# Kernel tuning notes

Measured on AMD Instinct MI355X. Metric: run time of the kernel, lower is better.

## Reference

```python
import jax, jax.numpy as jnp
import numpy as np


def setup_inputs() -> dict:
    key = jax.random.key(0)
    ks = jax.random.split(key, 13)
    B, T, D = 512, 256, 64
    H, G = 256, 192          # encoder hidden, lifted dim
    L = D + G                # ldim = 256
    s = lambda n: 1.0 / np.sqrt(n)
    return {
        "x": jax.random.normal(ks[0], (B, T, D), jnp.float32),
        "u": jax.random.normal(ks[1], (B, T, D), jnp.float32),
        "Wx1": jax.random.normal(ks[2], (D, H), jnp.float32) * s(D),
        "bx1": jax.random.normal(ks[3], (H,), jnp.float32) * 0.01,
        "Wx2": jax.random.normal(ks[4], (H, H), jnp.float32) * s(H),
        "bx2": jax.random.normal(ks[5], (H,), jnp.float32) * 0.01,
        "Wx3": jax.random.normal(ks[6], (H, G), jnp.float32) * s(H),
        "Wu1": jax.random.normal(ks[7], (D, H), jnp.float32) * s(D),
        "bu1": jax.random.normal(ks[8], (H,), jnp.float32) * 0.01,
        "Wu2": jax.random.normal(ks[9], (H, G), jnp.float32) * s(H),
        "WB": jax.random.normal(ks[10], (D + G, L), jnp.float32) * s(D + G),
        "WK": jax.random.normal(ks[11], (L, L), jnp.float32) * s(L),
        "bK": jax.random.normal(ks[12], (L,), jnp.float32) * 0.01,
        "n_shifts": 256,
    }


def reference(x, u, Wx1, bx1, Wx2, bx2, Wx3, Wu1, bu1, Wu2, WB, WK, bK, n_shifts):
    x = x[:, :n_shifts, :]
    u = u[:, :n_shifts, :]
    # encoder_x: relu(Linear) -> relu(Linear) -> Linear(no bias), dropout p=0 is identity
    g = jnp.maximum(x @ Wx1 + bx1, 0.0)
    g = jnp.maximum(g @ Wx2 + bx2, 0.0)
    g = g @ Wx3
    y = jnp.concatenate([x, g], axis=-1)          # [B, T, ldim]
    # encoder_u: relu(Linear) -> Linear(no bias)
    v = jnp.maximum(u @ Wu1 + bu1, 0.0) @ Wu2
    uu = jnp.concatenate([u, v], axis=-1)         # [B, T, D+G]
    Bu = uu @ WB                                  # [B, T, ldim]
    # Koopman linear recurrence: y_{t+1} = K y_t + bK + Bu_t
    y0 = y[:, 0, :]                               # [B, ldim]

    def step(carry, bu_t):
        y_next = carry @ WK + bK + bu_t
        return y_next, y_next

    _, ys = jax.lax.scan(step, y0, jnp.swapaxes(Bu[:, :-1, :], 0, 1))  # [T-1, B, ldim]
    y_pred = jnp.concatenate([y0[:, None, :], jnp.swapaxes(ys, 0, 1)], axis=1)
    return (y, y_pred)
```

## Files before the change

### kernel.cpp

```cpp
#include <hip/hip_runtime.h>
#include <hip/hip_bf16.h>

#define MM 131072

typedef __attribute__((ext_vector_type(8))) short short8;
typedef __attribute__((ext_vector_type(4))) float f32x4;

#define GLP(p) (const __attribute__((address_space(1))) void*)(p)
#define LDSP(p) (__attribute__((address_space(3))) void*)(p)

static __device__ __forceinline__ unsigned short f2bf(float f) {
    union { float f; unsigned int u; } v; v.f = f;
    unsigned int r = v.u + 0x7FFF + ((v.u >> 16) & 1);
    return (unsigned short)(r >> 16);
}
static __device__ __forceinline__ float bf2f(unsigned short h) {
    union { float f; unsigned int u; } v; v.u = ((unsigned int)h) << 16;
    return v.f;
}

__global__ __launch_bounds__(256) void prepA(
    const float* __restrict__ x, const float* __restrict__ u,
    __hip_bfloat16* __restrict__ xb, __hip_bfloat16* __restrict__ ub,
    float* __restrict__ y,
// ... 69 lines not shown
            __syncthreads();
            #pragma unroll
            for (int kk = 0; kk < 16; ++kk) {
                const float4 a4 = *(const float4*)&As[kk][ty * 4];
                const float4 w4 = *(const float4*)&Ws[kk][tx * 4];
                const float av[4] = {a4.x, a4.y, a4.z, a4.w};
                const float wv[4] = {w4.x, w4.y, w4.z, w4.w};
                #pragma unroll
                for (int i = 0; i < 4; ++i)
                    #pragma unroll
                    for (int j = 0; j < 4; ++j)
                        acc[i][j] += av[i] * wv[j];
            }
            __syncthreads();
        }
        #pragma unroll
        for (int i = 0; i < 4; ++i)
            #pragma unroll
            for (int j = 0; j < 4; ++j)
                C[(size_t)(row0 + ty * 4 + i) * 256 + col0 + tx * 4 + j] = acc[i][j];
    }
}

struct G5 { const float* a[5]; const float* b[5]; float* c[5]; };

__global__ __launch_bounds__(256) void wgemm(G5 P)
{
    __shared__ __align__(16) float As[16][68];
    __shared__ __align__(16) float Ws[16][64];

    const int e  = blockIdx.x >> 4;
    const int tl = blockIdx.x & 15;
    const float* A = P.a[e];
    const float* W = P.b[e];
    float*       C = P.c[e];
    const int row0 = (tl >> 2) * 64;
    const int col0 = (tl & 3) * 64;

    const int tx = threadIdx.x & 15;
    const int ty = threadIdx.x >> 4;

    float acc[4][4] = {};

    for (int k0 = 0; k0 < 256; k0 += 16) {
        {
            const int kk = threadIdx.x & 15;
            const int r  = threadIdx.x >> 4;
            #pragma unroll
            for (int rr = 0; rr < 4; ++rr)
                As[kk][r + rr * 16] = A[(size_t)(row0 + r + rr * 16) * 256 + k0 + kk];
        }
        {
            const int n  = threadIdx.x & 63;
            const int kz = threadIdx.x >> 6;
            #pragma unroll
            for (int kq = 0; kq < 4; ++kq) {
                const int kk = kz + kq * 4;
                Ws[kk][n] = W[(size_t)(k0 + kk) * 256 + col0 + n];
            }
        }
        __syncthreads();
        #pragma unroll
        for (int kk = 0; kk < 16; ++kk) {
            const float4 a4 = *(const float4*)&As[kk][ty * 4];
            const float4 w4 = *(const float4*)&Ws[kk][tx * 4];
            const float av[4] = {a4.x, a4.y, a4.z, a4.w};
            const float wv[4] = {w4.x, w4.y, w4.z, w4.w};
            #pragma unroll
            for (int i = 0; i < 4; ++i)
                #pragma unroll
                for (int j = 0; j < 4; ++j)
                    acc[i][j] += av[i] * wv[j];
        }
        __syncthreads();
    }

    #pragma unroll
    for (int i = 0; i < 4; ++i)
        #pragma unroll
        for (int j = 0; j < 4; ++j)
            C[(size_t)(row0 + ty * 4 + i) * 256 + col0 + tx * 4 + j] = acc[i][j];
}

__global__ __launch_bounds__(512) void ffC(
    const __hip_bfloat16* __restrict__ x_bf,
    const __hip_bfloat16* __restrict__ u_bf,
    const __hip_bfloat16* __restrict__ Wx1T, const float* __restrict__ bx1,
    const __hip_bfloat16* __restrict__ Wx2T, const float* __restrict__ bx2,
    const __hip_bfloat16* __restrict__ Wx3T,
    const __hip_bfloat16* __restrict__ Wu1T, const float* __restrict__ bu1,
    const __hip_bfloat16* __restrict__ Wu2T,
    float* __restrict__ y, __hip_bfloat16* __restrict__ vout,
    const float* __restrict__ WB, const float* __restrict__ WBW,
    const float* __restrict__ WBW2, const float* __restrict__ WBW3,
    __hip_bfloat16* __restrict__ T4,
    const float* __restrict__ bK, const float* __restrict__ WK,
    const float* __restrict__ W2f, const float* __restrict__ W3f,
    float* __restrict__ cK4)
{
    __shared__ __align__(16) __hip_bfloat16 I[128 * 256];
    __shared__ __align__(16) __hip_bfloat16 Bs[256 * 128];
    __shared__ __align__(16) __hip_bfloat16 As[128 * 64];

    const int tid  = threadIdx.x;

    if (blockIdx.x >= 2048) {
        if (blockIdx.x < 2560) {
            const int o = (blockIdx.x - 2048) * 512 + tid;
            const int n = o >> 10;
            const int rem = o & 1023;
            const int j = rem >> 8, k = rem & 255;
            const float* src = (j == 0) ? WB : (j == 1) ? WBW : (j == 2) ? WBW2 : WBW3;
            ((unsigned short*)T4)[o] = f2bf(src[(size_t)k * 256 + n]);
        } else {
            if (tid < 256) {
                const int col = tid;
                float s = bK[col];
                for (int k = 0; k < 256; ++k)
                    s += bK[k] * (WK[(size_t)k * 256 + col] + W2f[(size_t)k * 256 + col]
                                  + W3f[(size_t)k * 256 + col]);
                cK4[col] = s;
            }
        }
        return;
    }

    const bool isx = blockIdx.x < 1024;
    const __hip_bfloat16* in  = isx ? x_bf : u_bf;
    const __hip_bfloat16* W1T = isx ? Wx1T : Wu1T;
    const float*          b1  = isx ? bx1  : bu1;
    const int lane = tid & 63;
    const int wid  = tid >> 6;
    const int wm   = wid & 1;
    const int wn   = wid >> 1;
    const int row0 = (blockIdx.x & 1023) * 128;
    const int rlow = lane & 15;
    const int c    = lane >> 4;

    f32x4 acc[4][4];
    #pragma unroll
    for (int mi = 0; mi < 4; ++mi)
        #pragma unroll
        for (int ni = 0; ni < 4; ++ni)
            acc[mi][ni] = {0.f, 0.f, 0.f, 0.f};

    {
        #pragma unroll
        for (int r = 0; r < 2; ++r) {
            const int i = r * 512 + tid;
            const int row = i >> 3;
            const int cl  = (i & 7) ^ (row & 7);
            __builtin_amdgcn_global_load_lds(
                GLP(in + (size_t)(row0 + row) * 64 + cl * 8),
                LDSP(As + i * 8), 16, 0, 0);
        }
        #pragma unroll
        for (int r = 0; r < 4; ++r) {
            const int i = r * 512 + tid;
            const int row = i >> 3;
            const int cl  = (i & 7) ^ (row & 7);
            __builtin_amdgcn_global_load_lds(
                GLP(W1T + (size_t)row * 64 + cl * 8),
                LDSP(Bs + i * 8), 16, 0, 0);
        }
        __syncthreads();
        #pragma unroll
        for (int k0 = 0; k0 < 64; k0 += 32) {
            short8 af[4], bfr[4];
            #pragma unroll
            for (int mi = 0; mi < 4; ++mi) {
                const int row  = wm * 64 + mi * 16 + rlow;
                const int phys = ((k0 >> 3) + c) ^ (row & 7);
                af[mi] = *(const short8*)((const char*)As + row * 128 + phys * 16);
            }
            #pragma unroll
            for (int ni = 0; ni < 4; ++ni) {
                const int row  = wn * 64 + ni * 16 + rlow;
                const int phys = ((k0 >> 3) + c) ^ (row & 7);
                bfr[ni] = *(const short8*)((const char*)Bs + row * 128 + phys * 16);
            }
            #pragma unroll
            for (int mi = 0; mi < 4; ++mi)
                #pragma unroll
                for (int ni = 0; ni < 4; ++ni)
                    acc[mi][ni] = __builtin_amdgcn_mfma_f32_16x16x32_bf16(
                        af[mi], bfr[ni], acc[mi][ni], 0, 0, 0);
        }
        __syncthreads();
        #pragma unroll
        for (int ni = 0; ni < 4; ++ni) {
            const int col = wn * 64 + ni * 16 + rlow;
            const float bv = b1[col];
            #pragma unroll
            for (int q = 0; q < 4; ++q)
                #pragma unroll
                for (int mi = 0; mi < 4; ++mi) {
                    const int row = wm * 64 + mi * 16 + c * 4 + q;
                    const int byte = (row * 512 + col * 2) ^ ((row & 7) << 4);
                    *(unsigned short*)((char*)I + byte) = f2bf(fmaxf(acc[mi][ni][q] + bv, 0.f));
                }
        }
        __syncthreads();
    }

    if (isx) {
        #pragma unroll
        for (int mi = 0; mi < 4; ++mi)
            #pragma unroll
            for (int ni = 0; ni < 4; ++ni)
                acc[mi][ni] = {0.f, 0.f, 0.f, 0.f};

        for (int half = 0; half < 2; ++half) {
            const int k0b = half * 128;
            #pragma unroll
            for (int r = 0; r < 8; ++r) {
                const int i = r * 512 + tid;
                const int row = i >> 4;
                const int cl  = (i & 15) ^ (row & 7);
                __builtin_amdgcn_global_load_lds(
                    GLP(Wx2T + (size_t)row * 256 + k0b + cl * 8),
                    LDSP(Bs + i * 8), 16, 0, 0);
            }
            __syncthreads();
            #pragma unroll
            for (int k0l = 0; k0l < 128; k0l += 32) {
                short8 af[4], bfr[4];
                #pragma unroll
                for (int mi = 0; mi < 4; ++mi) {
                    const int row = wm * 64 + mi * 16 + rlow;
                    const int off = (row * 512 + (k0b + k0l) * 2 + c * 16) ^ ((row & 7) << 4);
                    af[mi] = *(const short8*)((const char*)I + off);
                }
                #pragma unroll
                for (int ni = 0; ni < 4; ++ni) {
                    const int row  = wn * 64 + ni * 16 + rlow;
                    const int phys = ((k0l >> 3) + c) ^ (row & 7);
                    bfr[ni] = *(const short8*)((const char*)Bs + row * 256 + phys * 16);
                }
                #pragma unroll
                for (int mi = 0; mi < 4; ++mi)
                    #pragma unroll
                    for (int ni = 0; ni < 4; ++ni)
                        acc[mi][ni] = __builtin_amdgcn_mfma_f32_16x16x32_bf16(
                            af[mi], bfr[ni], acc[mi][ni], 0, 0, 0);
            }
            __syncthreads();
        }
        #pragma unroll
        for (int ni = 0; ni < 4; ++ni) {
            const int col = wn * 64 + ni * 16 + rlow;
            const float bv = bx2[col];
            #pragma unroll
            for (int q = 0; q < 4; ++q)
                #pragma unroll
                for (int mi = 0; mi < 4; ++mi) {
                    const int row = wm * 64 + mi * 16 + c * 4 + q;
                    const int byte = (row * 512 + col * 2) ^ ((row & 7) << 4);
                    *(unsigned short*)((char*)I + byte) = f2bf(fmaxf(acc[mi][ni][q] + bv, 0.f));
                }
        }
        __syncthreads();
    }

    const __hip_bfloat16* WfT = isx ? Wx3T : Wu2T;
    f32x4 a3[4][3];
    #pragma unroll
    for (int mi = 0; mi < 4; ++mi)
        #pragma unroll
        for (int ni = 0; ni < 3; ++ni)
            a3[mi][ni] = {0.f, 0.f, 0.f, 0.f};

    for (int half = 0; half < 2; ++half) {
        const int k0b = half * 128;
        #pragma unroll
        for (int r = 0; r < 6; ++r) {
            const int i = r * 512 + tid;
            const int row = i >> 4;
            const int cl  = (i & 15) ^ (row & 7);
            __builtin_amdgcn_global_load_lds(
                GLP(WfT + (size_t)row * 256 + k0b + cl * 8),
                LDSP(Bs + i * 8), 16, 0, 0);
        }
        __syncthreads();
        #pragma unroll
        for (int k0l = 0; k0l < 128; k0l += 32) {
            short8 af[4], bfr[3];
            #pragma unroll
            for (int mi = 0; mi < 4; ++mi) {
                const int row = wm * 64 + mi * 16 + rlow;
                const int off = (row * 512 + (k0b + k0l) * 2 + c * 16) ^ ((row & 7) << 4);
                af[mi] = *(const short8*)((const char*)I + off);
            }
            #pragma unroll
            for (int ni = 0; ni < 3; ++ni) {
                const int row  = wn * 48 + ni * 16 + rlow;
                const int phys = ((k0l >> 3) + c) ^ (row & 7);
                bfr[ni] = *(const short8*)((const char*)Bs + row * 256 + phys * 16);
            }
            #pragma unroll
            for (int mi = 0; mi < 4; ++mi)
                #pragma unroll
                for (int ni = 0; ni < 3; ++ni)
                    a3[mi][ni] = __builtin_amdgcn_mfma_f32_16x16x32_bf16(
                        af[mi], bfr[ni], a3[mi][ni], 0, 0, 0);
        }
        __syncthreads();
    }
    #pragma unroll
    for (int ni = 0; ni < 3; ++ni) {
        const int col = wn * 48 + ni * 16 + rlow;
        #pragma unroll
        for (int mi = 0; mi < 4; ++mi)
            #pragma unroll
            for (int q = 0; q < 4; ++q) {
                const int row = row0 + wm * 64 + mi * 16 + c * 4 + q;
                if (isx) y[(size_t)row * 256 + 64 + col] = a3[mi][ni][q];
                else     ((unsigned short*)vout)[(size_t)row * 192 + col] = f2bf(a3[mi][ni][q]);
            }
    }
}

__global__ __launch_bounds__(256) void d4gS(
    const __hip_bfloat16* __restrict__ u_bf, const __hip_bfloat16* __restrict__ v,
    const __hip_bfloat16* __restrict__ WBT4, const float* __restrict__ cK4,
    float* __restrict__ yp,
    const __hip_bfloat16* __restrict__ WBT, const float* __restrict__ bK,
    float* __restrict__ stash)
{
    __shared__ __align__(16) __hip_bfloat16 As[132 * 32];
    __shared__ __align__(16) __hip_bfloat16 Bs[4][128 * 32];

    const int tid  = threadIdx.x;

    if (blockIdx.x >= 2048) {
        float* uuL = (float*)As;
        const int b = blockIdx.x - 2048;
        #pragma unroll
        for (int p = 0; p < 3; ++p) {
            float val;
            if (tid < 64) val = bf2f(((const unsigned short*)u_bf)[((size_t)b * 256 + p) * 64 + tid]);
            else          val = bf2f(((const unsigned short*)v)[((size_t)b * 256 + p) * 192 + tid - 64]);
            uuL[p * 256 + tid] = val;
        }
        __syncthreads();
        const int col = tid;
        float a0 = bK[col], a1 = a0, a2 = a0;
        for (int k = 0; k < 256; ++k) {
            const float w = bf2f(((const unsigned short*)WBT)[(size_t)col * 256 + k]);
            a0 += uuL[0 * 256 + k] * w;
            a1 += uuL[1 * 256 + k] * w;
            a2 += uuL[2 * 256 + k] * w;
        }
        stash[((size_t)b * 3 + 0) * 256 + col] = a0;
        stash[((size_t)b * 3 + 1) * 256 + col] = a1;
        stash[((size_t)b * 3 + 2) * 256 + col] = a2;
        return;
    }

    const int lane = tid & 63;
    const int wid  = tid >> 6;
    const int wm   = wid & 1;
    const int wn   = wid >> 1;
    const int row0 = (blockIdx.x >> 1) * 128;
    const int col0 = (blockIdx.x & 1) * 128;
    const int rlow = lane & 15;
    const int c    = lane >> 4;

    f32x4 acc[4][4];
    #pragma unroll
    for (int mi = 0; mi < 4; ++mi)
        #pragma unroll
        for (int ni = 0; ni < 4; ++ni)
            acc[mi][ni] = {0.f, 0.f, 0.f, 0.f};

    for (int kl = 0; kl < 256; kl += 32) {
        const __hip_bfloat16* Ab; int Al, kk;
        if (kl < 64) { Ab = u_bf; Al = 64;  kk = kl; }
        else         { Ab = v;    Al = 192; kk = kl - 64; }

        #pragma unroll
        for (int r = 0; r < 3; ++r) {
            const int i = r * 256 + tid;
            if (i < 528) {
                const int row = i >> 2;
                const int cl  = (i & 3) ^ ((row >> 1) & 3);
                int srow = row0 - 4 + row;
                if (srow < 0) srow = 0;
                __builtin_amdgcn_global_load_lds(
                    GLP(Ab + (size_t)srow * Al + kk + cl * 8),
                    LDSP(As + i * 8), 16, 0, 0);
            }
        }
        #pragma unroll
        for (int r = 0; r < 8; ++r) {
            const int i = r * 256 + tid;
            const int j = i >> 9;
            const int s = i & 511;
            const int row = s >> 2;
            const int cl  = (s & 3) ^ ((row >> 1) & 3);
            __builtin_amdgcn_global_load_lds(
                GLP(WBT4 + (size_t)(col0 + row) * 1024 + j * 256 + kl + cl * 8),
                LDSP(&Bs[0][0] + i * 8), 16, 0, 0);
        }
        __syncthreads();

        #pragma unroll
        for (int j = 0; j < 4; ++j) {
            short8 bfr[4];
            #pragma unroll
            for (int ni = 0; ni < 4; ++ni) {
                const int row  = wn * 64 + ni * 16 + rlow;
                const int phys = c ^ ((row >> 1) & 3);
                bfr[ni] = *(const short8*)((const char*)Bs[j] + row * 64 + phys * 16);
            }
            #pragma unroll
            for (int mi = 0; mi < 4; ++mi) {
                const int prow = wm * 64 + mi * 16 + rlow + 3 - j;
                const int phys = c ^ ((prow >> 1) & 3);
                const short8 af = *(const short8*)((const char*)As + prow * 64 + phys * 16);
                #pragma unroll
                for (int ni = 0; ni < 4; ++ni)
                    acc[mi][ni] = __builtin_amdgcn_mfma_f32_16x16x32_bf16(
                        af, bfr[ni], acc[mi][ni], 0, 0, 0);
            }
        }
        __syncthreads();
    }

    const int q4 = lane >> 4;
    #pragma unroll
    for (int ni = 0; ni < 4; ++ni) {
        const int col = col0 + wn * 64 + ni * 16 + rlow;
        const float bv = cK4[col];
        #pragma unroll
        for (int mi = 0; mi < 4; ++mi) {
            #pragma unroll
            for (int q = 0; q < 4; ++q) {
                const int row = row0 + wm * 64 + mi * 16 + q4 * 4 + q;
                if ((row & 255) >= 4)
                    yp[(size_t)row * 256 + col] = acc[mi][ni][q] + bv;
            }
        }
    }
}

static __device__ __forceinline__ void gather_frags(
    const float* __restrict__ M, int col0, int rlow, int kg,
    short8 (&wh)[2][8], short8 (&wl)[2][8])
{
    #pragma unroll
    for (int tile = 0; tile < 2; ++tile) {
        const int col = col0 + tile * 16 + rlow;
        for (int kc = 0; kc < 8; ++kc) {
            const int k0 = kc * 32 + kg * 8;
            short8 h, l;
            for (int i = 0; i < 8; ++i) {
                const float w = M[(size_t)(k0 + i) * 256 + col];
                const unsigned short hb = f2bf(w);
                h[i] = (short)hb;
                l[i] = (short)f2bf(w - bf2f(hb));
            }
            wh[tile][kc] = h;
            wl[tile][kc] = l;
        }
    }
}

__global__ __launch_bounds__(512, 1) void scan4(
    const float* __restrict__ WK, const float* __restrict__ W4,
    const float* __restrict__ stash,
    const float* __restrict__ y, float* __restrict__ yp)
{
    __shared__ __align__(16) __hip_bfloat16 cbuf[2][2][16 * 256];

    const int tid  = threadIdx.x;
    const int lane = tid & 63;
    const int wid  = tid >> 6;
    const int b0   = blockIdx.x * 4;
    const int col0 = wid * 32;
    const int rlow = lane & 15;
    const int kg   = lane >> 4;
    const int rswz = (rlow & 7) << 4;

    #pragma unroll
    for (int e = 0; e < 2; ++e) {
        const int idx = tid * 2 + e;
        const int br  = idx >> 8;
        const int cc  = idx & 255;
        const float v = y[(size_t)(b0 + br) * 65536 + cc];
        yp[(size_t)(b0 + br) * 65536 + cc] = v;
        const unsigned short hb = f2bf(v);
        const unsigned short lb = f2bf(v - bf2f(hb));
        const int byte = (br * 512 + cc * 2) ^ ((br & 7) << 4);
        *(unsigned short*)((char*)&cbuf[0][0][0] + byte) = hb;
        *(unsigned short*)((char*)&cbuf[0][1][0] + byte) = lb;
    }
    __syncthreads();

    short8 wh[2][8], wl[2][8];
    gather_frags(WK, col0, rlow, kg, wh, wl);

    for (int p = 1; p < 4; ++p) {
        f32x4 aHH[2], aHL[2], aLH[2], bHH[2], bHL[2], bLH[2];
        #pragma unroll
        for (int tile = 0; tile < 2; ++tile) {
            aHH[tile] = {0.f,0.f,0.f,0.f}; aHL[tile] = {0.f,0.f,0.f,0.f}; aLH[tile] = {0.f,0.f,0.f,0.f};
            bHH[tile] = {0.f,0.f,0.f,0.f}; bHL[tile] = {0.f,0.f,0.f,0.f}; bLH[tile] = {0.f,0.f,0.f,0.f};
        }
        const char* hbase = (const char*)&cbuf[0][0][0];
        const char* lbase = (const char*)&cbuf[0][1][0];
        #pragma unroll
        for (int kc = 0; kc < 4; ++kc) {
            const int off = (rlow * 512 + kg * 16 + kc * 64) ^ rswz;
            const short8 ah = *(const short8*)(hbase + off);
            const short8 al = *(const short8*)(lbase + off);
            aHH[0] = __builtin_amdgcn_mfma_f32_16x16x32_bf16(ah, wh[0][kc], aHH[0], 0, 0, 0);
            aHH[1] = __builtin_amdgcn_mfma_f32_16x16x32_bf16(ah, wh[1][kc], aHH[1], 0, 0, 0);
            aHL[0] = __builtin_amdgcn_mfma_f32_16x16x32_bf16(ah, wl[0][kc], aHL[0], 0, 0, 0);
            aHL[1] = __builtin_amdgcn_mfma_f32_16x16x32_bf16(ah, wl[1][kc], aHL[1], 0, 0, 0);
            aLH[0] = __builtin_amdgcn_mfma_f32_16x16x32_bf16(al, wh[0][kc], aLH[0], 0, 0, 0);
            aLH[1] = __builtin_amdgcn_mfma_f32_16x16x32_bf16(al, wh[1][kc], aLH[1], 0, 0, 0);
        }
        #pragma unroll
        for (int kc = 4; kc < 8; ++kc) {
            const int off = (rlow * 512 + kg * 16 + kc * 64) ^ rswz;
            const short8 ah = *(const short8*)(hbase + off);
            const short8 al = *(const short8*)(lbase + off);
            bHH[0] = __builtin_amdgcn_mfma_f32_16x16x32_bf16(ah, wh[0][kc], bHH[0], 0, 0, 0);
            bHH[1] = __builtin_amdgcn_mfma_f32_16x16x32_bf16(ah, wh[1][kc], bHH[1], 0, 0, 0);
            bHL[0] = __builtin_amdgcn_mfma_f32_16x16x32_bf16(ah, wl[0][kc], bHL[0], 0, 0, 0);
            bHL[1] = __builtin_amdgcn_mfma_f32_16x16x32_bf16(ah, wl[1][kc], bHL[1], 0, 0, 0);
            bLH[0] = __builtin_amdgcn_mfma_f32_16x16x32_bf16(al, wh[0][kc], bLH[0], 0, 0, 0);
            bLH[1] = __builtin_amdgcn_mfma_f32_16x16x32_bf16(al, wh[1][kc], bLH[1], 0, 0, 0);
        }
        __builtin_amdgcn_sched_barrier(0);
        asm volatile("s_waitcnt lgkmcnt(0)" ::: "memory");
        __builtin_amdgcn_s_barrier();
        __builtin_amdgcn_sched_barrier(0);

        if (kg == p - 1) {
            #pragma unroll
            for (int tile = 0; tile < 2; ++tile) {
                const int col = col0 + tile * 16 + rlow;
                #pragma unroll
                for (int q = 0; q < 4; ++q) {
                    const float cv = stash[((size_t)(b0 + q) * 3 + (p - 1)) * 256 + col];
                    const float yv = (aHH[tile][q] + bHH[tile][q]) + (aHL[tile][q] + bHL[tile][q])
                                   + (aLH[tile][q] + bLH[tile][q]) + cv;
                    const int wr = p * 4 + q;
                    const unsigned short hb = f2bf(yv);
                    const unsigned short lb = f2bf(yv - bf2f(hb));
                    const int byte = (wr * 512 + col * 2) ^ ((wr & 7) << 4);
                    *(unsigned short*)((char*)&cbuf[0][0][0] + byte) = hb;
                    *(unsigned short*)((char*)&cbuf[0][1][0] + byte) = lb;
                    yp[(size_t)(b0 + q) * 65536 + (size_t)p * 256 + col] = yv;
                }
            }
        }
        __builtin_amdgcn_sched_barrier(0);
        asm volatile("s_waitcnt lgkmcnt(0)" ::: "memory");
        __builtin_amdgcn_s_barrier();
        __builtin_amdgcn_sched_barrier(0);
    }

    gather_frags(W4, col0, rlow, kg, wh, wl);

    float dv[2][4];
    #pragma unroll
    for (int tile = 0; tile < 2; ++tile) {
        const int col = col0 + tile * 16 + rlow;
        #pragma unroll
        for (int q = 0; q < 4; ++q)
            dv[tile][q] = yp[(size_t)(b0 + q) * 65536 + (size_t)(4 + kg) * 256 + col];
    }

    int cur = 0;
    for (int s = 0; s < 63; ++s) {
        const int tb = 4 + s * 4;

        float dn[2][4];
        if (s < 62) {
            #pragma unroll
            for (int tile = 0; tile < 2; ++tile) {
                const int col = col0 + tile * 16 + rlow;
                #pragma unroll
                for (int q = 0; q < 4; ++q)
                    dn[tile][q] = yp[(size_t)(b0 + q) * 65536
                                     + (size_t)(tb + 4 + kg) * 256 + col];
            }
        }

        f32x4 aHH[2], aHL[2], aLH[2], bHH[2], bHL[2], bLH[2];
        #pragma unroll
        for (int tile = 0; tile < 2; ++tile) {
            aHH[tile] = {0.f,0.f,0.f,0.f}; aHL[tile] = {0.f,0.f,0.f,0.f}; aLH[tile] = {0.f,0.f,0.f,0.f};
            bHH[tile] = {0.f,0.f,0.f,0.f}; bHL[tile] = {0.f,0.f,0.f,0.f}; bLH[tile] = {0.f,0.f,0.f,0.f};
        }
        const char* hbase = (const char*)&cbuf[cur][0][0];
        const char* lbase = (const char*)&cbuf[cur][1][0];
        #pragma unroll
        for (int kc = 0; kc < 4; ++kc) {
            const int off = (rlow * 512 + kg * 16 + kc * 64) ^ rswz;
            const short8 ah = *(const short8*)(hbase + off);
            const short8 al = *(const short8*)(lbase + off);
            aHH[0] = __builtin_amdgcn_mfma_f32_16x16x32_bf16(ah, wh[0][kc], aHH[0], 0, 0, 0);
            aHH[1] = __builtin_amdgcn_mfma_f32_16x16x32_bf16(ah, wh[1][kc], aHH[1], 0, 0, 0);
            aHL[0] = __builtin_amdgcn_mfma_f32_16x16x32_bf16(ah, wl[0][kc], aHL[0], 0, 0, 0);
            aHL[1] = __builtin_amdgcn_mfma_f32_16x16x32_bf16(ah, wl[1][kc], aHL[1], 0, 0, 0);
            aLH[0] = __builtin_amdgcn_mfma_f32_16x16x32_bf16(al, wh[0][kc], aLH[0], 0, 0, 0);
            aLH[1] = __builtin_amdgcn_mfma_f32_16x16x32_bf16(al, wh[1][kc], aLH[1], 0, 0, 0);
        }
        #pragma unroll
        for (int kc = 4; kc < 8; ++kc) {
            const int off = (rlow * 512 + kg * 16 + kc * 64) ^ rswz;
            const short8 ah = *(const short8*)(hbase + off);
            const short8 al = *(const short8*)(lbase + off);
            bHH[0] = __builtin_amdgcn_mfma_f32_16x16x32_bf16(ah, wh[0][kc], bHH[0], 0, 0, 0);
            bHH[1] = __builtin_amdgcn_mfma_f32_16x16x32_bf16(ah, wh[1][kc], bHH[1], 0, 0, 0);
            bHL[0] = __builtin_amdgcn_mfma_f32_16x16x32_bf16(ah, wl[0][kc], bHL[0], 0, 0, 0);
            bHL[1] = __builtin_amdgcn_mfma_f32_16x16x32_bf16(ah, wl[1][kc], bHL[1], 0, 0, 0);
            bLH[0] = __builtin_amdgcn_mfma_f32_16x16x32_bf16(al, wh[0][kc], bLH[0], 0, 0, 0);
            bLH[1] = __builtin_amdgcn_mfma_f32_16x16x32_bf16(al, wh[1][kc], bLH[1], 0, 0, 0);
        }

        char* whb = (char*)&cbuf[cur ^ 1][0][0];
        char* wlb = (char*)&cbuf[cur ^ 1][1][0];
        #pragma unroll
        for (int tile = 0; tile < 2; ++tile) {
            const int col = col0 + tile * 16 + rlow;
            #pragma unroll
            for (int q = 0; q < 4; ++q) {
                const int row = kg * 4 + q;
                const float yv = (aHH[tile][q] + bHH[tile][q]) + (aHL[tile][q] + bHL[tile][q])
                               + (aLH[tile][q] + bLH[tile][q]) + dv[tile][q];
                const unsigned short hb = f2bf(yv);
                const unsigned short lb = f2bf(yv - bf2f(hb));
                const int byte = (row * 512 + col * 2) ^ ((row & 7) << 4);
                *(unsigned short*)(whb + byte) = hb;
                *(unsigned short*)(wlb + byte) = lb;
                yp[(size_t)(b0 + q) * 65536 + (size_t)(tb + kg) * 256 + col] = yv;
            }
        }
        if (s < 62) {
            #pragma unroll
            for (int tile = 0; tile < 2; ++tile)
                #pragma unroll
                for (int q = 0; q < 4; ++q)
                    dv[tile][q] = dn[tile][q];
        }

        __builtin_amdgcn_sched_barrier(0);
        asm volatile("s_waitcnt lgkmcnt(0)" ::: "memory");
        __builtin_amdgcn_s_barrier();
        __builtin_amdgcn_sched_barrier(0);
        cur ^= 1;
    }
}

extern "C" void kernel_launch(void* const* d_in, const int* in_sizes, int n_in,
                              void* d_out, int out_size, void* d_ws, size_t ws_size,
                              hipStream_t stream)
{
    const float* x   = (const float*)d_in[0];
    const float* u   = (const float*)d_in[1];
    const float* Wx1 = (const float*)d_in[2];
    const float* bx1 = (const float*)d_in[3];
    const float* Wx2 = (const float*)d_in[4];
    const float* bx2 = (const float*)d_in[5];
    const float* Wx3 = (const float*)d_in[6];
    const float* Wu1 = (const float*)d_in[7];
    const float* bu1 = (const float*)d_in[8];
    const float* Wu2 = (const float*)d_in[9];
    const float* WB  = (const float*)d_in[10];
    const float* WK  = (const float*)d_in[11];
    const float* bK  = (const float*)d_in[12];

    float* y  = (float*)d_out;
    float* yp = y + (size_t)MM * 256;

    char* ws = (char*)d_ws;
    __hip_bfloat16* x_bf = (__hip_bfloat16*)(ws);
    __hip_bfloat16* u_bf = (__hip_bfloat16*)(ws + 16777216);
    __hip_bfloat16* wTb  = (__hip_bfloat16*)(ws + 33554432);
    __hip_bfloat16* Wx1T = wTb;
    __hip_bfloat16* Wx2T = wTb + 16384;
    __hip_bfloat16* Wx3T = wTb + 81920;
    __hip_bfloat16* Wu1T = wTb + 131072;
    __hip_bfloat16* Wu2T = wTb + 147456;
    __hip_bfloat16* WBT  = wTb + 196608;
    __hip_bfloat16* t2   = (__hip_bfloat16*)(ws + 34078720);
    float* W2f   = (float*)(ws + 101187584);
    float* W3f   = (float*)(ws + 101449728);
    float* W4f   = (float*)(ws + 101711872);
    float* WBWf  = (float*)(ws + 101974016);
    float* WBW2f = (float*)(ws + 102236160);
    float* WBW3f = (float*)(ws + 102498304);
    __hip_bfloat16* WBT4 = (__hip_bfloat16*)(ws + 102760448);
    float* cK4   = (float*)(ws + 103284736);
    float* stash = (float*)(ws + 103285760);

    prepA<<<17440, dim3(256), 0, stream>>>(x, u, x_bf, u_bf, y,
        Wx1, Wx2, Wx3, Wu1, Wu2, WB,
        Wx1T, Wx2T, Wx3T, Wu1T, Wu2T, WBT,
        WK, WB, W2f, WBWf);

    {
        G5 L2 = {{W2f, W2f, WBWf, WBWf, nullptr},
                 {WK, W2f, WK, W2f, nullptr},
                 {W3f, W4f, WBW2f, WBW3f, nullptr}};
        wgemm<<<64, dim3(256), 0, stream>>>(L2);
    }

    ffC<<<2561, dim3(512), 0, stream>>>(x_bf, u_bf,
        Wx1T, bx1, Wx2T, bx2, Wx3T, Wu1T, bu1, Wu2T,
        y, t2,
        WB, WBWf, WBW2f, WBW3f, WBT4,
        bK, WK, W2f, W3f, cK4);

    d4gS<<<2560, dim3(256), 0, stream>>>(u_bf, t2, WBT4, cK4, yp, WBT, bK, stash);

    scan4<<<128, dim3(512), 0, stream>>>(WK, W4f, stash, y, yp);
}
```

Baseline: 392.7 us.

## Overlap x-encoder MLP with Koopman scan by moving it into scan kernel

```diff
diff --git a/kernel.cpp b/kernel.cpp
--- a/kernel.cpp
+++ b/kernel.cpp
@@ -175,7 +175,204 @@
             C[(size_t)(row0 + ty * 4 + i) * 256 + col0 + tx * 4 + j] = acc[i][j];
 }
 
-__global__ __launch_bounds__(512) void ffC(
+static __device__ void ffx_impl(
+    const __hip_bfloat16* __restrict__ x_bf,
+    const __hip_bfloat16* __restrict__ W1T, const float* __restrict__ b1,
+    const __hip_bfloat16* __restrict__ W2T, const float* __restrict__ b2,
+    const __hip_bfloat16* __restrict__ W3T,
+    float* __restrict__ y, int row0, int rs, char* smem, int tid)
+{
+    __hip_bfloat16* I  = (__hip_bfloat16*)smem;
+    __hip_bfloat16* Bs = (__hip_bfloat16*)(smem + 65536);
+    __hip_bfloat16* As = (__hip_bfloat16*)(smem + 131072);
+
+    const int lane = tid & 63;
+    const int wid  = tid >> 6;
+    const int wm   = wid & 1;
+    const int wn   = wid >> 1;
+    const int rlow = lane & 15;
+    const int c    = lane >> 4;
+
+    f32x4 acc[4][4];
+    #pragma unroll
+    for (int mi = 0; mi < 4; ++mi)
+        #pragma unroll
+        for (int ni = 0; ni < 4; ++ni)
+            acc[mi][ni] = {0.f, 0.f, 0.f, 0.f};
+
+    {
+        #pragma unroll
+        for (int r = 0; r < 2; ++r) {
+            const int i = r * 512 + tid;
+            const int row = i >> 3;
+            const int cl  = (i & 7) ^ (row & 7);
+            __builtin_amdgcn_global_load_lds(
+                GLP(x_bf + (size_t)(row0 + row * rs) * 64 + cl * 8),
+                LDSP(As + i * 8), 16, 0, 0);
+        }
+        #pragma unroll
+        for (int r = 0; r < 4; ++r) {
+            const int i = r * 512 + tid;
+            const int row = i >> 3;
+            const int cl  = (i & 7) ^ (row & 7);
+            __builtin_amdgcn_global_load_lds(
+                GLP(W1T + (size_t)row * 64 + cl * 8),
+                LDSP(Bs + i * 8), 16, 0, 0);
+        }
+        __syncthreads();
+        #pragma unroll
+        for (int k0 = 0; k0 < 64; k0 += 32) {
+            short8 af[4], bfr[4];
+            #pragma unroll
+            for (int mi = 0; mi < 4; ++mi) {
+                const int row  = wm * 64 + mi * 16 + rlow;
+                const int phys = ((k0 >> 3) + c) ^ (row & 7);
+                af[mi] = *(const short8*)((const char*)As + row * 128 + phys * 16);
+            }
+            #pragma unroll
+            for (int ni = 0; ni < 4; ++ni) {
+                const int row  = wn * 64 + ni * 16 + rlow;
+                const int phys = ((k0 >> 3) + c) ^ (row & 7);
+                bfr[ni] = *(const short8*)((const char*)Bs + row * 128 + phys * 16);
+            }
+            #pragma unroll
+            for (int mi = 0; mi < 4; ++mi)
+                #pragma unroll
+                for (int ni = 0; ni < 4; ++ni)
+                    acc[mi][ni] = __builtin_amdgcn_mfma_f32_16x16x32_bf16(
+                        af[mi], bfr[ni], acc[mi][ni], 0, 0, 0);
+        }
+        __syncthreads();
+        #pragma unroll
+        for (int ni = 0; ni < 4; ++ni) {
+            const int col = wn * 64 + ni * 16 + rlow;
+            const float bv = b1[col];
+            #pragma unroll
+            for (int q = 0; q < 4; ++q)
+                #pragma unroll
+                for (int mi = 0; mi < 4; ++mi) {
+                    const int row = wm * 64 + mi * 16 + c * 4 + q;
+                    const int byte = (row * 512 + col * 2) ^ ((row & 7) << 4);
+                    *(unsigned short*)((char*)I + byte) = f2bf(fmaxf(acc[mi][ni][q] + bv, 0.f));
+                }
+        }
+        __syncthreads();
+    }
+
+    #pragma unroll
+    for (int mi = 0; mi < 4; ++mi)
+        #pragma unroll
+        for (int ni = 0; ni < 4; ++ni)
+            acc[mi][ni] = {0.f, 0.f, 0.f, 0.f};
+
+    for (int half = 0; half < 2; ++half) {
+        const int k0b = half * 128;
+        #pragma unroll
+        for (int r = 0; r < 8; ++r) {
+            const int i = r * 512 + tid;
+            const int row = i >> 4;
+            const int cl  = (i & 15) ^ (row & 7);
+            __builtin_amdgcn_global_load_lds(
+                GLP(W2T + (size_t)row * 256 + k0b + cl * 8),
+                LDSP(Bs + i * 8), 16, 0, 0);
+        }
+        __syncthreads();
+        #pragma unroll
+        for (int k0l = 0; k0l < 128; k0l += 32) {
+            short8 af[4], bfr[4];
+            #pragma unroll
+            for (int mi = 0; mi < 4; ++mi) {
+                const int row = wm * 64 + mi * 16 + rlow;
+                const int off = (row * 512 + (k0b + k0l) * 2 + c * 16) ^ ((row & 7) << 4);
+                af[mi] = *(const short8*)((const char*)I + off);
+            }
+            #pragma unroll
+            for (int ni = 0; ni < 4; ++ni) {
+                const int row  = wn * 64 + ni * 16 + rlow;
+                const int phys = ((k0l >> 3) + c) ^ (row & 7);
+                bfr[ni] = *(const short8*)((const char*)Bs + row * 256 + phys * 16);
+            }
+            #pragma unroll
+            for (int mi = 0; mi < 4; ++mi)
+                #pragma unroll
+                for (int ni = 0; ni < 4; ++ni)
+                    acc[mi][ni] = __builtin_amdgcn_mfma_f32_16x16x32_bf16(
+                        af[mi], bfr[ni], acc[mi][ni], 0, 0, 0);
+        }
+        __syncthreads();
+    }
+    #pragma unroll
+    for (int ni = 0; ni < 4; ++ni) {
+        const int col = wn * 64 + ni * 16 + rlow;
+        const float bv = b2[col];
+        #pragma unroll
+        for (int q = 0; q < 4; ++q)
+            #pragma unroll
+            for (int mi = 0; mi < 4; ++mi) {
+                const int row = wm * 64 + mi * 16 + c * 4 + q;
+                const int byte = (row * 512 + col * 2) ^ ((row & 7) << 4);
+                *(unsigned short*)((char*)I + byte) = f2bf(fmaxf(acc[mi][ni][q] + bv, 0.f));
+            }
+    }
+    __syncthreads();
+
+    f32x4 a3[4][3];
+    #pragma unroll
+    for (int mi = 0; mi < 4; ++mi)
+        #pragma unroll
+        for (int ni = 0; ni < 3; ++ni)
+            a3[mi][ni] = {0.f, 0.f, 0.f, 0.f};
+
+    for (int half = 0; half < 2; ++half) {
+        const int k0b = half * 128;
+        #pragma unroll
+        for (int r = 0; r < 6; ++r) {
+            const int i = r * 512 + tid;
+            const int row = i >> 4;
+            const int cl  = (i & 15) ^ (row & 7);
+            __builtin_amdgcn_global_load_lds(
+                GLP(W3T + (size_t)row * 256 + k0b + cl * 8),
+                LDSP(Bs + i * 8), 16, 0, 0);
+        }
+        __syncthreads();
+        #pragma unroll
+        for (int k0l = 0; k0l < 128; k0l += 32) {
+            short8 af[4], bfr[3];
+            #pragma unroll
+            for (int mi = 0; mi < 4; ++mi) {
+                const int row = wm * 64 + mi * 16 + rlow;
+                const int off = (row * 512 + (k0b + k0l) * 2 + c * 16) ^ ((row & 7) << 4);
+                af[mi] = *(const short8*)((const char*)I + off);
+            }
+            #pragma unroll
+            for (int ni = 0; ni < 3; ++ni) {
+                const int row  = wn * 48 + ni * 16 + rlow;
+                const int phys = ((k0l >> 3) + c) ^ (row & 7);
+                bfr[ni] = *(const short8*)((const char*)Bs + row * 256 + phys * 16);
+            }
+            #pragma unroll
+            for (int mi = 0; mi < 4; ++mi)
+                #pragma unroll
+                for (int ni = 0; ni < 3; ++ni)
+                    a3[mi][ni] = __builtin_amdgcn_mfma_f32_16x16x32_bf16(
+                        af[mi], bfr[ni], a3[mi][ni], 0, 0, 0);
+        }
+        __syncthreads();
+    }
+    #pragma unroll
+    for (int ni = 0; ni < 3; ++ni) {
+        const int col = wn * 48 + ni * 16 + rlow;
+        #pragma unroll
+        for (int mi = 0; mi < 4; ++mi)
+            #pragma unroll
+            for (int q = 0; q < 4; ++q) {
+                const int row = row0 + (wm * 64 + mi * 16 + c * 4 + q) * rs;
+                y[(size_t)row * 256 + 64 + col] = a3[mi][ni][q];
+            }
+    }
+}
+
+__global__ __launch_bounds__(512) void midC(
     const __hip_bfloat16* __restrict__ x_bf,
     const __hip_bfloat16* __restrict__ u_bf,
     const __hip_bfloat16* __restrict__ Wx1T, const float* __restrict__ bx1,
@@ -191,21 +388,18 @@
     const float* __restrict__ W2f, const float* __restrict__ W3f,
     float* __restrict__ cK4)
 {
-    __shared__ __align__(16) __hip_bfloat16 I[128 * 256];
-    __shared__ __align__(16) __hip_bfloat16 Bs[256 * 128];
-    __shared__ __align__(16) __hip_bfloat16 As[128 * 64];
-
-    const int tid  = threadIdx.x;
-
-    if (blockIdx.x >= 2048) {
-        if (blockIdx.x < 2560) {
-            const int o = (blockIdx.x - 2048) * 512 + tid;
+    __shared__ __align__(16) char smem[147456];
+    const int tid = threadIdx.x;
+
+    if (blockIdx.x >= 1024) {
+        if (blockIdx.x < 1536) {
+            const int o = (blockIdx.x - 1024) * 512 + tid;
             const int n = o >> 10;
             const int rem = o & 1023;
             const int j = rem >> 8, k = rem & 255;
             const float* src = (j == 0) ? WB : (j == 1) ? WBW : (j == 2) ? WBW2 : WBW3;
             ((unsigned short*)T4)[o] = f2bf(src[(size_t)k * 256 + n]);
-        } else {
+        } else if (blockIdx.x == 1536) {
             if (tid < 256) {
                 const int col = tid;
                 float s = bK[col];
@@ -214,19 +408,23 @@
                                   + W3f[(size_t)k * 256 + col]);
                 cK4[col] = s;
             }
+        } else {
+            const int base = (blockIdx.x - 1537) * 128;
+            ffx_impl(x_bf, Wx1T, bx1, Wx2T, bx2, Wx3T, y,
+                     base * 256, 256, smem, tid);
         }
         return;
     }
 
-    const bool isx = blockIdx.x < 1024;
-    const __hip_bfloat16* in  = isx ? x_bf : u_bf;
-    const __hip_bfloat16* W1T = isx ? Wx1T : Wu1T;
-    const float*          b1  = isx ? bx1  : bu1;
+    __hip_bfloat16* I  = (__hip_bfloat16*)smem;
+    __hip_bfloat16* Bs = (__hip_bfloat16*)(smem + 65536);
+    __hip_bfloat16* As = (__hip_bfloat16*)(smem + 131072);
+
     const int lane = tid & 63;
     const int wid  = tid >> 6;
     const int wm   = wid & 1;
     const int wn   = wid >> 1;
-    const int row0 = (blockIdx.x & 1023) * 128;
+    const int row0 = blockIdx.x * 128;
     const int rlow = lane & 15;
     const int c    = lane >> 4;
 
@@ -244,7 +442,7 @@
             const int row = i >> 3;
             const int cl  = (i & 7) ^ (row & 7);
             __builtin_amdgcn_global_load_lds(
-                GLP(in + (size_t)(row0 + row) * 64 + cl * 8),
+                GLP(u_bf + (size_t)(row0 + row) * 64 + cl * 8),
                 LDSP(As + i * 8), 16, 0, 0);
         }
         #pragma unroll
@@ -253,7 +451,7 @@
             const int row = i >> 3;
             const int cl  = (i & 7) ^ (row & 7);
             __builtin_amdgcn_global_load_lds(
-                GLP(W1T + (size_t)row * 64 + cl * 8),
+                GLP(Wu1T + (size_t)row * 64 + cl * 8),
                 LDSP(Bs + i * 8), 16, 0, 0);
         }
         __syncthreads();
@@ -283,7 +481,7 @@
         #pragma unroll
         for (int ni = 0; ni < 4; ++ni) {
             const int col = wn * 64 + ni * 16 + rlow;
-            const float bv = b1[col];
+            const float bv = bu1[col];
             #pragma unroll
             for (int q = 0; q < 4; ++q)
                 #pragma unroll
@@ -296,66 +494,6 @@
         __syncthreads();
     }
 
-    if (isx) {
-        #pragma unroll
-        for (int mi = 0; mi < 4; ++mi)
-            #pragma unroll
-            for (int ni = 0; ni < 4; ++ni)
-                acc[mi][ni] = {0.f, 0.f, 0.f, 0.f};
-
-        for (int half = 0; half < 2; ++half) {
-            const int k0b = half * 128;
-            #pragma unroll
-            for (int r = 0; r < 8; ++r) {
-                const int i = r * 512 + tid;
-                const int row = i >> 4;
-                const int cl  = (i & 15) ^ (row & 7);
-                __builtin_amdgcn_global_load_lds(
-                    GLP(Wx2T + (size_t)row * 256 + k0b + cl * 8),
-                    LDSP(Bs + i * 8), 16, 0, 0);
-            }
-            __syncthreads();
-            #pragma unroll
-            for (int k0l = 0; k0l < 128; k0l += 32) {
-                short8 af[4], bfr[4];
-                #pragma unroll
-                for (int mi = 0; mi < 4; ++mi) {
-                    const int row = wm * 64 + mi * 16 + rlow;
-                    const int off = (row * 512 + (k0b + k0l) * 2 + c * 16) ^ ((row & 7) << 4);
-                    af[mi] = *(const short8*)((const char*)I + off);
-                }
-                #pragma unroll
-                for (int ni = 0; ni < 4; ++ni) {
-                    const int row  = wn * 64 + ni * 16 + rlow;
-                    const int phys = ((k0l >> 3) + c) ^ (row & 7);
-                    bfr[ni] = *(const short8*)((const char*)Bs + row * 256 + phys * 16);
-                }
-                #pragma unroll
-                for (int mi = 0; mi < 4; ++mi)
-                    #pragma unroll
-                    for (int ni = 0; ni < 4; ++ni)
-                        acc[mi][ni] = __builtin_amdgcn_mfma_f32_16x16x32_bf16(
-                            af[mi], bfr[ni], acc[mi][ni], 0, 0, 0);
-            }
-            __syncthreads();
-        }
-        #pragma unroll
-        for (int ni = 0; ni < 4; ++ni) {
-            const int col = wn * 64 + ni * 16 + rlow;
-            const float bv = bx2[col];
-            #pragma unroll
-            for (int q = 0; q < 4; ++q)
-                #pragma unroll
-                for (int mi = 0; mi < 4; ++mi) {
-                    const int row = wm * 64 + mi * 16 + c * 4 + q;
-                    const int byte = (row * 512 + col * 2) ^ ((row & 7) << 4);
-                    *(unsigned short*)((char*)I + byte) = f2bf(fmaxf(acc[mi][ni][q] + bv, 0.f));
-                }
-        }
-        __syncthreads();
-    }
-
-    const __hip_bfloat16* WfT = isx ? Wx3T : Wu2T;
     f32x4 a3[4][3];
     #pragma unroll
     for (int mi = 0; mi < 4; ++mi)
@@ -371,7 +509,7 @@
             const int row = i >> 4;
             const int cl  = (i & 15) ^ (row & 7);
             __builtin_amdgcn_global_load_lds(
-                GLP(WfT + (size_t)row * 256 + k0b + cl * 8),
+                GLP(Wu2T + (size_t)row * 256 + k0b + cl * 8),
                 LDSP(Bs + i * 8), 16, 0, 0);
         }
         __syncthreads();
@@ -407,8 +545,7 @@
             #pragma unroll
             for (int q = 0; q < 4; ++q) {
                 const int row = row0 + wm * 64 + mi * 16 + c * 4 + q;
-                if (isx) y[(size_t)row * 256 + 64 + col] = a3[mi][ni][q];
-                else     ((unsigned short*)vout)[(size_t)row * 192 + col] = f2bf(a3[mi][ni][q]);
+                ((unsigned short*)vout)[(size_t)row * 192 + col] = f2bf(a3[mi][ni][q]);
             }
     }
 }
@@ -559,14 +696,28 @@
     }
 }
 
-__global__ __launch_bounds__(512, 1) void scan4(
+__global__ __launch_bounds__(512, 1) void scanFX(
     const float* __restrict__ WK, const float* __restrict__ W4,
     const float* __restrict__ stash,
-    const float* __restrict__ y, float* __restrict__ yp)
+    const float* __restrict__ y, float* __restrict__ yp,
+    const __hip_bfloat16* __restrict__ x_bf,
+    const __hip_bfloat16* __restrict__ Wx1T, const float* __restrict__ bx1,
+    const __hip_bfloat16* __restrict__ Wx2T, const float* __restrict__ bx2,
+    const __hip_bfloat16* __restrict__ Wx3T,
+    float* __restrict__ yob)
 {
-    __shared__ __align__(16) __hip_bfloat16 cbuf[2][2][16 * 256];
-
+    __shared__ __align__(16) char smem[147456];
     const int tid  = threadIdx.x;
+
+    if (blockIdx.x >= 128) {
+        ffx_impl(x_bf, Wx1T, bx1, Wx2T, bx2, Wx3T, yob,
+                 (blockIdx.x - 128) * 128, 1, smem, tid);
+        return;
+    }
+
+    typedef __hip_bfloat16 CB[2][16 * 256];
+    CB* cbuf = (CB*)smem;
+
     const int lane = tid & 63;
     const int wid  = tid >> 6;
     const int b0   = blockIdx.x * 4;
@@ -804,7 +955,7 @@
         wgemm<<<64, dim3(256), 0, stream>>>(L2);
     }
 
-    ffC<<<2561, dim3(512), 0, stream>>>(x_bf, u_bf,
+    midC<<<1541, dim3(512), 0, stream>>>(x_bf, u_bf,
         Wx1T, bx1, Wx2T, bx2, Wx3T, Wu1T, bu1, Wu2T,
         y, t2,
         WB, WBWf, WBW2f, WBW3f, WBT4,
@@ -812,5 +963,6 @@
 
     d4gS<<<2560, dim3(256), 0, stream>>>(u_bf, t2, WBT4, cK4, yp, WBT, bK, stash);
 
-    scan4<<<128, dim3(512), 0, stream>>>(WK, W4f, stash, y, yp);
+    scanFX<<<1152, dim3(512), 0, stream>>>(WK, W4f, stash, y, yp,
+        x_bf, Wx1T, bx1, Wx2T, bx2, Wx3T, y);
 }
```

Result: slower. 414.2 us (+5.5%).

## Split scan4 across 16 waves with one 16-column tile each

Applied to the files above, without the earlier changes.

```diff
diff --git a/kernel.cpp b/kernel.cpp
--- a/kernel.cpp
+++ b/kernel.cpp
@@ -537,29 +537,26 @@
     }
 }
 
-static __device__ __forceinline__ void gather_frags(
+static __device__ __forceinline__ void gather_frags1(
     const float* __restrict__ M, int col0, int rlow, int kg,
-    short8 (&wh)[2][8], short8 (&wl)[2][8])
+    short8 (&wh)[8], short8 (&wl)[8])
 {
-    #pragma unroll
-    for (int tile = 0; tile < 2; ++tile) {
-        const int col = col0 + tile * 16 + rlow;
-        for (int kc = 0; kc < 8; ++kc) {
-            const int k0 = kc * 32 + kg * 8;
-            short8 h, l;
-            for (int i = 0; i < 8; ++i) {
-                const float w = M[(size_t)(k0 + i) * 256 + col];
-                const unsigned short hb = f2bf(w);
-                h[i] = (short)hb;
-                l[i] = (short)f2bf(w - bf2f(hb));
-            }
-            wh[tile][kc] = h;
-            wl[tile][kc] = l;
-        }
-    }
-}
-
-__global__ __launch_bounds__(512, 1) void scan4(
+    const int col = col0 + rlow;
+    for (int kc = 0; kc < 8; ++kc) {
+        const int k0 = kc * 32 + kg * 8;
+        short8 h, l;
+        for (int i = 0; i < 8; ++i) {
+            const float w = M[(size_t)(k0 + i) * 256 + col];
+            const unsigned short hb = f2bf(w);
+            h[i] = (short)hb;
+            l[i] = (short)f2bf(w - bf2f(hb));
+        }
+        wh[kc] = h;
+        wl[kc] = l;
+    }
+}
+
+__global__ __launch_bounds__(1024, 1) void scan4(
     const float* __restrict__ WK, const float* __restrict__ W4,
     const float* __restrict__ stash,
     const float* __restrict__ y, float* __restrict__ yp)
@@ -570,16 +567,14 @@
     const int lane = tid & 63;
     const int wid  = tid >> 6;
     const int b0   = blockIdx.x * 4;
-    const int col0 = wid * 32;
+    const int col0 = wid * 16;
     const int rlow = lane & 15;
     const int kg   = lane >> 4;
     const int rswz = (rlow & 7) << 4;
 
-    #pragma unroll
-    for (int e = 0; e < 2; ++e) {
-        const int idx = tid * 2 + e;
-        const int br  = idx >> 8;
-        const int cc  = idx & 255;
+    {
+        const int br = tid >> 8;
+        const int cc = tid & 255;
         const float v = y[(size_t)(b0 + br) * 65536 + cc];
         yp[(size_t)(b0 + br) * 65536 + cc] = v;
         const unsigned short hb = f2bf(v);
@@ -590,41 +585,21 @@
     }
     __syncthreads();
 
-    short8 wh[2][8], wl[2][8];
-    gather_frags(WK, col0, rlow, kg, wh, wl);
+    short8 wh[8], wl[8];
+    gather_frags1(WK, col0, rlow, kg, wh, wl);
 
     for (int p = 1; p < 4; ++p) {
-        f32x4 aHH[2], aHL[2], aLH[2], bHH[2], bHL[2], bLH[2];
-        #pragma unroll
-        for (int tile = 0; tile < 2; ++tile) {
-            aHH[tile] = {0.f,0.f,0.f,0.f}; aHL[tile] = {0.f,0.f,0.f,0.f}; aLH[tile] = {0.f,0.f,0.f,0.f};
-            bHH[tile] = {0.f,0.f,0.f,0.f}; bHL[tile] = {0.f,0.f,0.f,0.f}; bLH[tile] = {0.f,0.f,0.f,0.f};
-        }
+        f32x4 aHH = {0.f,0.f,0.f,0.f}, aHL = {0.f,0.f,0.f,0.f}, aLH = {0.f,0.f,0.f,0.f};
         const char* hbase = (const char*)&cbuf[0][0][0];
         const char* lbase = (const char*)&cbuf[0][1][0];
         #pragma unroll
-        for (int kc = 0; kc < 4; ++kc) {
+        for (int kc = 0; kc < 8; ++kc) {
             const int off = (rlow * 512 + kg * 16 + kc * 64) ^ rswz;
             const short8 ah = *(const short8*)(hbase + off);
             const short8 al = *(const short8*)(lbase + off);
-            aHH[0] = __builtin_amdgcn_mfma_f32_16x16x32_bf16(ah, wh[0][kc], aHH[0], 0, 0, 0);
-            aHH[1] = __builtin_amdgcn_mfma_f32_16x16x32_bf16(ah, wh[1][kc], aHH[1], 0, 0, 0);
-            aHL[0] = __builtin_amdgcn_mfma_f32_16x16x32_bf16(ah, wl[0][kc], aHL[0], 0, 0, 0);
-            aHL[1] = __builtin_amdgcn_mfma_f32_16x16x32_bf16(ah, wl[1][kc], aHL[1], 0, 0, 0);
-            aLH[0] = __builtin_amdgcn_mfma_f32_16x16x32_bf16(al, wh[0][kc], aLH[0], 0, 0, 0);
-            aLH[1] = __builtin_amdgcn_mfma_f32_16x16x32_bf16(al, wh[1][kc], aLH[1], 0, 0, 0);
-        }
-        #pragma unroll
-        for (int kc = 4; kc < 8; ++kc) {
-            const int off = (rlow * 512 + kg * 16 + kc * 64) ^ rswz;
-            const short8 ah = *(const short8*)(hbase + off);
-            const short8 al = *(const short8*)(lbase + off);
-            bHH[0] = __builtin_amdgcn_mfma_f32_16x16x32_bf16(ah, wh[0][kc], bHH[0], 0, 0, 0);
-            bHH[1] = __builtin_amdgcn_mfma_f32_16x16x32_bf16(ah, wh[1][kc], bHH[1], 0, 0, 0);
-            bHL[0] = __builtin_amdgcn_mfma_f32_16x16x32_bf16(ah, wl[0][kc], bHL[0], 0, 0, 0);
-            bHL[1] = __builtin_amdgcn_mfma_f32_16x16x32_bf16(ah, wl[1][kc], bHL[1], 0, 0, 0);
-            bLH[0] = __builtin_amdgcn_mfma_f32_16x16x32_bf16(al, wh[0][kc], bLH[0], 0, 0, 0);
-            bLH[1] = __builtin_amdgcn_mfma_f32_16x16x32_bf16(al, wh[1][kc], bLH[1], 0, 0, 0);
+            aHH = __builtin_amdgcn_mfma_f32_16x16x32_bf16(ah, wh[kc], aHH, 0, 0, 0);
+            aHL = __builtin_amdgcn_mfma_f32_16x16x32_bf16(ah, wl[kc], aHL, 0, 0, 0);
+            aLH = __builtin_amdgcn_mfma_f32_16x16x32_bf16(al, wh[kc], aLH, 0, 0, 0);
         }
         __builtin_amdgcn_sched_barrier(0);
         asm volatile("s_waitcnt lgkmcnt(0)" ::: "memory");
@@ -632,22 +607,18 @@
         __builtin_amdgcn_sched_barrier(0);
 
         if (kg == p - 1) {
-            #pragma unroll
-            for (int tile = 0; tile < 2; ++tile) {
-                const int col = col0 + tile * 16 + rlow;
-                #pragma unroll
-                for (int q = 0; q < 4; ++q) {
-                    const float cv = stash[((size_t)(b0 + q) * 3 + (p - 1)) * 256 + col];
-                    const float yv = (aHH[tile][q] + bHH[tile][q]) + (aHL[tile][q] + bHL[tile][q])
-                                   + (aLH[tile][q] + bLH[tile][q]) + cv;
-                    const int wr = p * 4 + q;
-                    const unsigned short hb = f2bf(yv);
-                    const unsigned short lb = f2bf(yv - bf2f(hb));
-                    const int byte = (wr * 512 + col * 2) ^ ((wr & 7) << 4);
-                    *(unsigned short*)((char*)&cbuf[0][0][0] + byte) = hb;
-                    *(unsigned short*)((char*)&cbuf[0][1][0] + byte) = lb;
-                    yp[(size_t)(b0 + q) * 65536 + (size_t)p * 256 + col] = yv;
-                }
+            const int col = col0 + rlow;
+            #pragma unroll
+            for (int q = 0; q < 4; ++q) {
+                const float cv = stash[((size_t)(b0 + q) * 3 + (p - 1)) * 256 + col];
+                const float yv = aHH[q] + aHL[q] + aLH[q] + cv;
+                const int wr = p * 4 + q;
+                const unsigned short hb = f2bf(yv);
+                const unsigned short lb = f2bf(yv - bf2f(hb));
+                const int byte = (wr * 512 + col * 2) ^ ((wr & 7) << 4);
+                *(unsigned short*)((char*)&cbuf[0][0][0] + byte) = hb;
+                *(unsigned short*)((char*)&cbuf[0][1][0] + byte) = lb;
+                yp[(size_t)(b0 + q) * 65536 + (size_t)p * 256 + col] = yv;
             }
         }
         __builtin_amdgcn_sched_barrier(0);
@@ -656,76 +627,50 @@
         __builtin_amdgcn_sched_barrier(0);
     }
 
-    gather_frags(W4, col0, rlow, kg, wh, wl);
-
-    float dv[2][4];
-    #pragma unroll
-    for (int tile = 0; tile < 2; ++tile) {
-        const int col = col0 + tile * 16 + rlow;
+    gather_frags1(W4, col0, rlow, kg, wh, wl);
+
+    float dv[4];
+    {
+        const int col = col0 + rlow;
         #pragma unroll
         for (int q = 0; q < 4; ++q)
-            dv[tile][q] = yp[(size_t)(b0 + q) * 65536 + (size_t)(4 + kg) * 256 + col];
+            dv[q] = yp[(size_t)(b0 + q) * 65536 + (size_t)(4 + kg) * 256 + col];
     }
 
     int cur = 0;
     for (int s = 0; s < 63; ++s) {
         const int tb = 4 + s * 4;
 
-        float dn[2][4];
+        float dn[4];
         if (s < 62) {
-            #pragma unroll
-            for (int tile = 0; tile < 2; ++tile) {
-                const int col = col0 + tile * 16 + rlow;
-                #pragma unroll
-                for (int q = 0; q < 4; ++q)
-                    dn[tile][q] = yp[(size_t)(b0 + q) * 65536
-                                     + (size_t)(tb + 4 + kg) * 256 + col];
-            }
-        }
-
-        f32x4 aHH[2], aHL[2], aLH[2], bHH[2], bHL[2], bLH[2];
-        #pragma unroll
-        for (int tile = 0; tile < 2; ++tile) {
-            aHH[tile] = {0.f,0.f,0.f,0.f}; aHL[tile] = {0.f,0.f,0.f,0.f}; aLH[tile] = {0.f,0.f,0.f,0.f};
-            bHH[tile] = {0.f,0.f,0.f,0.f}; bHL[tile] = {0.f,0.f,0.f,0.f}; bLH[tile] = {0.f,0.f,0.f,0.f};
-        }
+            const int col = col0 + rlow;
+            #pragma unroll
+            for (int q = 0; q < 4; ++q)
+                dn[q] = yp[(size_t)(b0 + q) * 65536
+                           + (size_t)(tb + 4 + kg) * 256 + col];
+        }
+
+        f32x4 aHH = {0.f,0.f,0.f,0.f}, aHL = {0.f,0.f,0.f,0.f}, aLH = {0.f,0.f,0.f,0.f};
         const char* hbase = (const char*)&cbuf[cur][0][0];
         const char* lbase = (const char*)&cbuf[cur][1][0];
         #pragma unroll
-        for (int kc = 0; kc < 4; ++kc) {
+        for (int kc = 0; kc < 8; ++kc) {
             const int off = (rlow * 512 + kg * 16 + kc * 64) ^ rswz;
             const short8 ah = *(const short8*)(hbase + off);
             const short8 al = *(const short8*)(lbase + off);
-            aHH[0] = __builtin_amdgcn_mfma_f32_16x16x32_bf16(ah, wh[0][kc], aHH[0], 0, 0, 0);
-            aHH[1] = __builtin_amdgcn_mfma_f32_16x16x32_bf16(ah, wh[1][kc], aHH[1], 0, 0, 0);
-            aHL[0] = __builtin_amdgcn_mfma_f32_16x16x32_bf16(ah, wl[0][kc], aHL[0], 0, 0, 0);
-            aHL[1] = __builtin_amdgcn_mfma_f32_16x16x32_bf16(ah, wl[1][kc], aHL[1], 0, 0, 0);
-            aLH[0] = __builtin_amdgcn_mfma_f32_16x16x32_bf16(al, wh[0][kc], aLH[0], 0, 0, 0);
-            aLH[1] = __builtin_amdgcn_mfma_f32_16x16x32_bf16(al, wh[1][kc], aLH[1], 0, 0, 0);
-        }
-        #pragma unroll
-        for (int kc = 4; kc < 8; ++kc) {
-            const int off = (rlow * 512 + kg * 16 + kc * 64) ^ rswz;
-            const short8 ah = *(const short8*)(hbase + off);
-            const short8 al = *(const short8*)(lbase + off);
-            bHH[0] = __builtin_amdgcn_mfma_f32_16x16x32_bf16(ah, wh[0][kc], bHH[0], 0, 0, 0);
-            bHH[1] = __builtin_amdgcn_mfma_f32_16x16x32_bf16(ah, wh[1][kc], bHH[1], 0, 0, 0);
-            bHL[0] = __builtin_amdgcn_mfma_f32_16x16x32_bf16(ah, wl[0][kc], bHL[0], 0, 0, 0);
-            bHL[1] = __builtin_amdgcn_mfma_f32_16x16x32_bf16(ah, wl[1][kc], bHL[1], 0, 0, 0);
-            bLH[0] = __builtin_amdgcn_mfma_f32_16x16x32_bf16(al, wh[0][kc], bLH[0], 0, 0, 0);
-            bLH[1] = __builtin_amdgcn_mfma_f32_16x16x32_bf16(al, wh[1][kc], bLH[1], 0, 0, 0);
+            aHH = __builtin_amdgcn_mfma_f32_16x16x32_bf16(ah, wh[kc], aHH, 0, 0, 0);
+            aHL = __builtin_amdgcn_mfma_f32_16x16x32_bf16(ah, wl[kc], aHL, 0, 0, 0);
+            aLH = __builtin_amdgcn_mfma_f32_16x16x32_bf16(al, wh[kc], aLH, 0, 0, 0);
         }
 
         char* whb = (char*)&cbuf[cur ^ 1][0][0];
         char* wlb = (char*)&cbuf[cur ^ 1][1][0];
-        #pragma unroll
-        for (int tile = 0; tile < 2; ++tile) {
-            const int col = col0 + tile * 16 + rlow;
+        {
+            const int col = col0 + rlow;
             #pragma unroll
             for (int q = 0; q < 4; ++q) {
                 const int row = kg * 4 + q;
-                const float yv = (aHH[tile][q] + bHH[tile][q]) + (aHL[tile][q] + bHL[tile][q])
-                               + (aLH[tile][q] + bLH[tile][q]) + dv[tile][q];
+                const float yv = aHH[q] + aHL[q] + aLH[q] + dv[q];
                 const unsigned short hb = f2bf(yv);
                 const unsigned short lb = f2bf(yv - bf2f(hb));
                 const int byte = (row * 512 + col * 2) ^ ((row & 7) << 4);
@@ -736,10 +681,8 @@
         }
         if (s < 62) {
             #pragma unroll
-            for (int tile = 0; tile < 2; ++tile)
-                #pragma unroll
-                for (int q = 0; q < 4; ++q)
-                    dv[tile][q] = dn[tile][q];
+            for (int q = 0; q < 4; ++q)
+                dv[q] = dn[q];
         }
 
         __builtin_amdgcn_sched_barrier(0);
@@ -812,5 +755,5 @@
 
     d4gS<<<2560, dim3(256), 0, stream>>>(u_bf, t2, WBT4, cK4, yp, WBT, bK, stash);
 
-    scan4<<<128, dim3(512), 0, stream>>>(WK, W4f, stash, y, yp);
-}
+    scan4<<<128, dim3(1024), 0, stream>>>(WK, W4f, stash, y, yp);
+}
```

Result: slower. 402.4 us (+2.5%).
